# Performance work log

Measured on AMD Instinct MI355X. Metric: run time of the kernel, lower is better.

The kernel has to match this reference:

```python
import jax, jax.numpy as jnp
import numpy as np

EPS = 1e-5

def _ligru_layer(x, W, U, gamma, beta):
    # x: [B,T,F]; W: [2H,F]; U: [2H,H]; gamma/beta: [2H]
    B, T, _ = x.shape
    H = U.shape[1]
    w = jnp.einsum('btf,hf->bth', x, W)            # [B,T,2H] input projection
    # BatchNorm1d (training mode) over flattened (B*T, 2H)
    wf = w.reshape(B * T, 2 * H)
    mu = wf.mean(axis=0)
    var = wf.var(axis=0)
    wf = (wf - mu) / jnp.sqrt(var + EPS) * gamma + beta
    w = wf.reshape(B, T, 2 * H)

    Ut = U.T                                       # [H,2H]

    def step(h, wt):
        uh = h @ Ut                                # [B,2H]
        m = uh.mean(axis=-1, keepdims=True)
        v = uh.var(axis=-1, keepdims=True)
        uh = (uh - m) / jnp.sqrt(v + EPS)          # LayerNorm, no affine
        gates = wt + uh
        at, zt = gates[:, :H], gates[:, H:]
        zt = jax.nn.sigmoid(zt)
        h = zt * h + (1.0 - zt) * jax.nn.relu(at)
        return h, h

    h0 = jnp.zeros((B, H), x.dtype)
    _, hs = jax.lax.scan(step, h0, jnp.swapaxes(w, 0, 1))  # [T,B,H]
    return jnp.swapaxes(hs, 0, 1)                          # [B,T,H]


def setup_inputs() -> dict:
    key = jax.random.key(0)
    ks = jax.random.split(key, 5)
    B, T, F, H = 32, 1000, 80, 1024
    x = jax.random.normal(ks[0], (B, T, F), dtype=jnp.float32)
    W1 = jax.random.normal(ks[1], (2 * H, F), dtype=jnp.float32) * 0.05
    U1 = jax.random.normal(ks[2], (2 * H, H), dtype=jnp.float32) * 0.03
    W2 = jax.random.normal(ks[3], (2 * H, H), dtype=jnp.float32) * 0.03
    U2 = jax.random.normal(ks[4], (2 * H, H), dtype=jnp.float32) * 0.03
    g = jnp.ones((2 * H,), jnp.float32)
    b = jnp.zeros((2 * H,), jnp.float32)
    return {"x": x, "W1": W1, "U1": U1, "g1": g, "b1": b,
            "W2": W2, "U2": U2, "g2": g, "b2": b}


def reference(x, W1, U1, g1, b1, W2, U2, g2, b2):
    h = _ligru_layer(x, W1, U1, g1, b1)
    h = _ligru_layer(h, W2, U2, g2, b2)
    return h
```

## Files before the change

kernel.cpp:

```cpp
#include <hip/hip_runtime.h>

typedef unsigned short u16;
typedef _Float16 f16;
typedef f16 half8 __attribute__((ext_vector_type(8)));
typedef float float4v __attribute__((ext_vector_type(4)));

union HV { uint4 u; half8 h; u16 s[8]; };

__device__ __forceinline__ float h2f(u16 u) { union { u16 u; f16 h; } c; c.u = u; return (float)c.h; }
__device__ __forceinline__ u16 f2h(float f) { union { u16 u; f16 h; } c; c.h = (f16)f; return c.u; }

__device__ __forceinline__ void store_coh_u16(u16* p, unsigned v) {
  asm volatile("global_store_short %0, %1, off sc0 sc1" :: "v"(p), "v"(v) : "memory");
}
__device__ __forceinline__ void store_coh_u32(void* p, unsigned v) {
  asm volatile("global_store_dword %0, %1, off sc0 sc1" :: "v"(p), "v"(v) : "memory");
}
__device__ __forceinline__ void store_coh_f32_tag(float* p, float val, unsigned tag) {
  unsigned long long pk = (unsigned long long)__float_as_uint(val) |
                          ((unsigned long long)tag << 32);
  asm volatile("global_store_dwordx2 %0, %1, off sc0 sc1" :: "v"(p), "v"(pk) : "memory");
}

__global__ void cvt_f32_f16(const float* __restrict__ s, u16* __restrict__ d, int n) {
  for (int i = blockIdx.x * blockDim.x + threadIdx.x; i < n; i += gridDim.x * blockDim.x)
    d[i] = f2h(s[i]);
}

__global__ __launch_bounds__(256) void gemm_f16(const u16* __restrict__ A, const u16* __restrict__ B,
                                                u16* __restrict__ C, int K) {
  __shared__ u16 As[128][40];
  __shared__ u16 Bs[128][40];
  const int tid = threadIdx.x, lane = tid & 63, wid = tid >> 6;
  const int col = lane & 15, quad = lane >> 4;
  const int wm = (wid & 1) * 64, wn = (wid >> 1) * 64;
  const int n0 = blockIdx.x * 128;
  const int m0 = blockIdx.y * 128;
  float4v acc[4][4];
  #pragma unroll
  for (int i = 0; i < 4; ++i)
    #pragma unroll
    for (int j = 0; j < 4; ++j) acc[i][j] = (float4v){0.f, 0.f, 0.f, 0.f};

  const int srow = tid >> 2;
  const int schunk = (tid & 3) * 8;

  for (int k0 = 0; k0 < K; k0 += 32) {
    __syncthreads();
    #pragma unroll
    for (int r2 = 0; r2 < 2; ++r2) {
      int row = srow + 64 * r2;
      int kk = k0 + schunk;
      uint4 av = {0, 0, 0, 0}, bv = {0, 0, 0, 0};
      if (kk + 8 <= K) {
        av = *(const uint4*)(A + (size_t)(m0 + row) * K + kk);
        bv = *(const uint4*)(B + (size_t)(n0 + row) * K + kk);
      }
      *(uint4*)&As[row][schunk] = av;
      *(uint4*)&Bs[row][schunk] = bv;
    }
    __syncthreads();
    HV af[4], bf[4];
    #pragma unroll
    for (int i = 0; i < 4; ++i) af[i].u = *(const uint4*)&As[wm + i * 16 + col][quad * 8];
    #pragma unroll
    for (int j = 0; j < 4; ++j) bf[j].u = *(const uint4*)&Bs[wn + j * 16 + col][quad * 8];
    #pragma unroll
    for (int i = 0; i < 4; ++i)
      #pragma unroll
      for (int j = 0; j < 4; ++j)
        acc[i][j] = __builtin_amdgcn_mfma_f32_16x16x32_f16(af[i].h, bf[j].h, acc[i][j], 0, 0, 0);
  }
  #pragma unroll
  for (int i = 0; i < 4; ++i)
    #pragma unroll
    for (int j = 0; j < 4; ++j)
      #pragma unroll
      for (int r = 0; r < 4; ++r) {
        int m = m0 + wm + i * 16 + quad * 4 + r;
        int n = n0 + wn + j * 16 + col;
        C[(size_t)m * 2048 + n] = f2h(acc[i][j][r]);
      }
}

__global__ void bn_stats(const u16* __restrict__ C, float* __restrict__ acc) {
  int c = blockIdx.x * 256 + threadIdx.x;
  int r0 = blockIdx.y * 256;
  float s = 0.f, q = 0.f;
  for (int r = r0; r < r0 + 256; ++r) {
    float v = h2f(C[(size_t)r * 2048 + c]);
    s += v; q += v * v;
  }
  atomicAdd(&acc[2 * c], s);
  atomicAdd(&acc[2 * c + 1], q);
}

__global__ void bn_final(const float* __restrict__ acc, const float* __restrict__ g,
                         const float* __restrict__ b, float2* __restrict__ ss) {
  int c = blockIdx.x * 256 + threadIdx.x;
  float mean = acc[2 * c] * (1.f / 32000.f);
  float var = acc[2 * c + 1] * (1.f / 32000.f) - mean * mean;
  float sc = g[c] * rsqrtf(var + 1e-5f);
  float2 o; o.x = sc; o.y = b[c] - mean * sc;
  ss[c] = o;
}

template <int OUT_F32>
__global__ __launch_bounds__(256, 1) void rec_kernel(
    const u16* __restrict__ w,
    const float2* __restrict__ ss,
    const u16* __restrict__ U,
    u16* hbuf,
    float* pstats,
    unsigned* flags,
    u16* out16, float* out32) {
  const int tid = threadIdx.x, lane = tid & 63, kh = tid >> 6;
  const int d = blockIdx.x >> 5, beta = blockIdx.x & 31;
  const int col = lane & 15, quad = lane >> 4;
  __shared__ float4v red[3][4][64];

  const int ja = beta * 32 + col;

  HV ufA0[8], ufA1[8], ufZ0[8], ufZ1[8];
  #pragma unroll
  for (int kk = 0; kk < 8; ++kk) {
    int k = kh * 256 + kk * 32 + quad * 8;
    ufA0[kk].u = *(const uint4*)(U + (size_t)ja * 1024 + k);
    ufA1[kk].u = *(const uint4*)(U + (size_t)(ja + 16) * 1024 + k);
    ufZ0[kk].u = *(const uint4*)(U + (size_t)(1024 + ja) * 1024 + k);
    ufZ1[kk].u = *(const uint4*)(U + (size_t)(1024 + ja + 16) * 1024 + k);
  }
  float2 ssA0 = ss[ja], ssA1 = ss[ja + 16];
  float2 ssZ0 = ss[1024 + ja], ssZ1 = ss[1024 + ja + 16];

  u16* hb = hbuf + (size_t)d * 16 * 1024;
  float* ps = pstats + (size_t)d * 4096;
  unsigned* f2 = flags + (size_t)d * 512;

  const u16* aptr = hb + (size_t)col * 1024 + kh * 256 + quad * 8;
  const int bloc = quad * 4;

  float hreg[4][2] = {{0.f, 0.f}, {0.f, 0.f}, {0.f, 0.f}, {0.f, 0.f}};
  u16 wa0[4], wa1[4], wz0[4], wz1[4];
  if (kh == 0) {
    #pragma unroll
    for (int r = 0; r < 4; ++r) {
      const u16* wr = w + ((size_t)(d * 16 + bloc + r) * 1000 + 0) * 2048 + ja;
      wa0[r] = wr[0]; wa1[r] = wr[16]; wz0[r] = wr[1024]; wz1[r] = wr[1040];
    }
  }

  for (int t = 0; t < 1000; ++t) {
    const unsigned tag = (unsigned)t + 1u;
    HV af[8];
    asm volatile(
        "global_load_dwordx4 %0, %8, off sc0 sc1\n\t"
        "global_load_dwordx4 %1, %8, off offset:64  sc0 sc1\n\t"
        "global_load_dwordx4 %2, %8, off offset:128 sc0 sc1\n\t"
        "global_load_dwordx4 %3, %8, off offset:192 sc0 sc1\n\t"
        "global_load_dwordx4 %4, %8, off offset:256 sc0 sc1\n\t"
        "global_load_dwordx4 %5, %8, off offset:320 sc0 sc1\n\t"
        "global_load_dwordx4 %6, %8, off offset:384 sc0 sc1\n\t"
        "global_load_dwordx4 %7, %8, off offset:448 sc0 sc1\n\t"
        "s_waitcnt vmcnt(0)"
        : "=v"(af[0].u), "=v"(af[1].u), "=v"(af[2].u), "=v"(af[3].u),
          "=v"(af[4].u), "=v"(af[5].u), "=v"(af[6].u), "=v"(af[7].u)
        : "v"(aptr)
        : "memory");

    float4v aA0 = (float4v){0.f, 0.f, 0.f, 0.f};
    float4v aA1 = (float4v){0.f, 0.f, 0.f, 0.f};
    float4v aZ0 = (float4v){0.f, 0.f, 0.f, 0.f};
    float4v aZ1 = (float4v){0.f, 0.f, 0.f, 0.f};
    #pragma unroll
    for (int kk = 0; kk < 8; ++kk) {
      aA0 = __builtin_amdgcn_mfma_f32_16x16x32_f16(af[kk].h, ufA0[kk].h, aA0, 0, 0, 0);
      aA1 = __builtin_amdgcn_mfma_f32_16x16x32_f16(af[kk].h, ufA1[kk].h, aA1, 0, 0, 0);
      aZ0 = __builtin_amdgcn_mfma_f32_16x16x32_f16(af[kk].h, ufZ0[kk].h, aZ0, 0, 0, 0);
      aZ1 = __builtin_amdgcn_mfma_f32_16x16x32_f16(af[kk].h, ufZ1[kk].h, aZ1, 0, 0, 0);
    }
    if (kh) {
      red[kh - 1][0][lane] = aA0; red[kh - 1][1][lane] = aA1;
      red[kh - 1][2][lane] = aZ0; red[kh - 1][3][lane] = aZ1;
    }
    __syncthreads();

    if (kh == 0) {
      aA0 += red[0][0][lane] + red[1][0][lane] + red[2][0][lane];
      aA1 += red[0][1][lane] + red[1][1][lane] + red[2][1][lane];
      aZ0 += red[0][2][lane] + red[1][2][lane] + red[2][2][lane];
      aZ1 += red[0][3][lane] + red[1][3][lane] + red[2][3][lane];
      const int p = t & 1;
      #pragma unroll
      for (int r = 0; r < 4; ++r) {
        float sv = aA0[r] + aA1[r] + aZ0[r] + aZ1[r];
        float qv = aA0[r] * aA0[r] + aA1[r] * aA1[r] + aZ0[r] * aZ0[r] + aZ1[r] * aZ1[r];
        #pragma unroll
        for (int off = 1; off < 16; off <<= 1) {
          sv += __shfl_xor(sv, off, 64);
          qv += __shfl_xor(qv, off, 64);
        }
        if (col == 0) {
          float* dst = ps + (((size_t)p * 16 + bloc + r) * 32 + beta) * 4;
          store_coh_f32_tag(dst, sv, tag);
          store_coh_f32_tag(dst + 2, qv, tag);
        }
      }
      u16 wn_a0[4], wn_a1[4], wn_z0[4], wn_z1[4];
      {
        int tn = t < 999 ? t + 1 : t;
        #pragma unroll
        for (int r = 0; r < 4; ++r) {
          const u16* wr = w + ((size_t)(d * 16 + bloc + r) * 1000 + tn) * 2048 + ja;
          wn_a0[r] = wr[0]; wn_a1[r] = wr[16]; wn_z0[r] = wr[1024]; wn_z1[r] = wr[1040];
        }
      }
      float4v g[8];
      const float* rb = ps + ((size_t)p * 16 + bloc) * 128 + col * 4;
      int ok;
      do {
        asm volatile(
            "global_load_dwordx4 %0, %8, off sc0 sc1\n\t"
            "global_load_dwordx4 %1, %8, off offset:256  sc0 sc1\n\t"
            "global_load_dwordx4 %2, %8, off offset:512  sc0 sc1\n\t"
            "global_load_dwordx4 %3, %8, off offset:768  sc0 sc1\n\t"
            "global_load_dwordx4 %4, %8, off offset:1024 sc0 sc1\n\t"
            "global_load_dwordx4 %5, %8, off offset:1280 sc0 sc1\n\t"
            "global_load_dwordx4 %6, %8, off offset:1536 sc0 sc1\n\t"
            "global_load_dwordx4 %7, %8, off offset:1792 sc0 sc1\n\t"
            "s_waitcnt vmcnt(0)"
            : "=v"(g[0]), "=v"(g[1]), "=v"(g[2]), "=v"(g[3]),
              "=v"(g[4]), "=v"(g[5]), "=v"(g[6]), "=v"(g[7])
            : "v"(rb)
            : "memory");
        int okl = 1;
        #pragma unroll
        for (int i = 0; i < 8; ++i)
          okl &= (__float_as_uint(g[i][1]) == tag && __float_as_uint(g[i][3]) == tag) ? 1 : 0;
        ok = __all(okl);
      } while (!ok);

      #pragma unroll
      for (int r = 0; r < 4; ++r) {
        float sm = g[2 * r][0] + g[2 * r + 1][0];
        float sq = g[2 * r][2] + g[2 * r + 1][2];
        #pragma unroll
        for (int off = 1; off < 16; off <<= 1) {
          sm += __shfl_xor(sm, off, 64);
          sq += __shfl_xor(sq, off, 64);
        }
        float mean = sm * (1.f / 2048.f);
        float var = sq * (1.f / 2048.f) - mean * mean;
        float inv = rsqrtf(var + 1e-5f);
        float ga0 = h2f(wa0[r]) * ssA0.x + ssA0.y + (aA0[r] - mean) * inv;
        float ga1 = h2f(wa1[r]) * ssA1.x + ssA1.y + (aA1[r] - mean) * inv;
        float gz0 = h2f(wz0[r]) * ssZ0.x + ssZ0.y + (aZ0[r] - mean) * inv;
        float gz1 = h2f(wz1[r]) * ssZ1.x + ssZ1.y + (aZ1[r] - mean) * inv;
        float z0 = 1.f / (1.f + __expf(-gz0));
        float z1 = 1.f / (1.f + __expf(-gz1));
        float h0 = z0 * hreg[r][0] + (1.f - z0) * (ga0 > 0.f ? ga0 : 0.f);
        float h1 = z1 * hreg[r][1] + (1.f - z1) * (ga1 > 0.f ? ga1 : 0.f);
        hreg[r][0] = h0; hreg[r][1] = h1;
        u16* hp = hb + (size_t)(bloc + r) * 1024 + ja;
        store_coh_u16(hp, (unsigned)f2h(h0));
        store_coh_u16(hp + 16, (unsigned)f2h(h1));
      }
      #pragma unroll
      for (int r = 0; r < 4; ++r) {
        wa0[r] = wn_a0[r]; wa1[r] = wn_a1[r];
        wz0[r] = wn_z0[r]; wz1[r] = wn_z1[r];
      }
      asm volatile("s_waitcnt vmcnt(0)" ::: "memory");
      if (lane == 0) store_coh_u32(f2 + (size_t)beta * 16, tag);
      #pragma unroll
      for (int r = 0; r < 4; ++r) {
        size_t orow = ((size_t)(d * 16 + bloc + r) * 1000 + t) * 1024 + ja;
        if (OUT_F32) { out32[orow] = hreg[r][0]; out32[orow + 16] = hreg[r][1]; }
        else         { out16[orow] = f2h(hreg[r][0]); out16[orow + 16] = f2h(hreg[r][1]); }
      }
    }
    {
      unsigned fv = tag; int ok;
      do {
        if (lane < 32)
          asm volatile("global_load_dword %0, %1, off sc0 sc1\n\ts_waitcnt vmcnt(0)"
                       : "=v"(fv) : "v"(f2 + (size_t)lane * 16) : "memory");
        ok = __all(lane < 32 ? (int)(fv >= tag) : 1);
      } while (!ok);
    }
  }
}

extern "C" void kernel_launch(void* const* d_in, const int* in_sizes, int n_in,
                              void* d_out, int out_size, void* d_ws, size_t ws_size,
                              hipStream_t stream) {
  (void)in_sizes; (void)n_in; (void)out_size;
  const float* x  = (const float*)d_in[0];
  const float* W1 = (const float*)d_in[1];
  const float* U1 = (const float*)d_in[2];
  const float* g1 = (const float*)d_in[3];
  const float* b1 = (const float*)d_in[4];
  const float* W2 = (const float*)d_in[5];
  const float* U2 = (const float*)d_in[6];
  const float* g2 = (const float*)d_in[7];
  const float* b2 = (const float*)d_in[8];

  char* ws = (char*)d_ws;
  size_t o = 0;
  auto take = [&](size_t bytes) { size_t r = o; o = (o + bytes + 255) & ~(size_t)255; return r; };
  u16* wbuf  = (u16*)(ws + take(32000ULL * 2048 * 2));
  u16* h1seq = (u16*)(ws + take(32000ULL * 1024 * 2));
  u16* xb    = (u16*)(ws + take(32000ULL * 80 * 2));
  u16* W1b   = (u16*)(ws + take(2048ULL * 80 * 2));
  u16* W2b   = (u16*)(ws + take(2048ULL * 1024 * 2));
  u16* U1b   = (u16*)(ws + take(2048ULL * 1024 * 2));
  u16* U2b   = (u16*)(ws + take(2048ULL * 1024 * 2));
  float2* ss1 = (float2*)(ws + take(2048 * 8));
  float2* ss2 = (float2*)(ws + take(2048 * 8));
  size_t zbase = o;
  float* acc1 = (float*)(ws + take(2048 * 8));
  float* acc2 = (float*)(ws + take(2048 * 8));
  float* pstats1 = (float*)(ws + take(2ULL * 2 * 16 * 32 * 4 * 4));
  float* pstats2 = (float*)(ws + take(2ULL * 2 * 16 * 32 * 4 * 4));
  unsigned* flags1 = (unsigned*)(ws + take(2ULL * 32 * 16 * 4));
  unsigned* flags2 = (unsigned*)(ws + take(2ULL * 32 * 16 * 4));
  u16* hbuf1 = (u16*)(ws + take(32 * 1024 * 2));
  u16* hbuf2 = (u16*)(ws + take(32 * 1024 * 2));
  size_t zlen = o - zbase;
  if (ws_size < o) return;

  (void)hipMemsetAsync(ws + zbase, 0, zlen, stream);

  cvt_f32_f16<<<1280, 256, 0, stream>>>(x, xb, 32000 * 80);
  cvt_f32_f16<<<160, 256, 0, stream>>>(W1, W1b, 2048 * 80);
  cvt_f32_f16<<<1024, 256, 0, stream>>>(U1, U1b, 2048 * 1024);
  cvt_f32_f16<<<1024, 256, 0, stream>>>(W2, W2b, 2048 * 1024);
  cvt_f32_f16<<<1024, 256, 0, stream>>>(U2, U2b, 2048 * 1024);

  gemm_f16<<<dim3(16, 250), 256, 0, stream>>>(xb, W1b, wbuf, 80);
  bn_stats<<<dim3(8, 125), 256, 0, stream>>>(wbuf, acc1);
  bn_final<<<8, 256, 0, stream>>>(acc1, g1, b1, ss1);
  rec_kernel<0><<<64, 256, 0, stream>>>(wbuf, ss1, U1b, hbuf1, pstats1, flags1, h1seq, nullptr);

  gemm_f16<<<dim3(16, 250), 256, 0, stream>>>(h1seq, W2b, wbuf, 1024);
  bn_stats<<<dim3(8, 125), 256, 0, stream>>>(wbuf, acc2);
  bn_final<<<8, 256, 0, stream>>>(acc2, g2, b2, ss2);
  rec_kernel<1><<<64, 256, 0, stream>>>(wbuf, ss2, U2b, hbuf2, pstats2, flags2, nullptr, (float*)d_out);
}
```

Before: 12.95 ms.

## Spread recurrent epilogue across all four waves instead of wave zero

Each of the four waves now stores its partial MFMA accumulators to shared memory and all-reduces them, so every wave holds the full sums. Each wave then handles the LayerNorm stats, gate math, h update and output stores for one quad of four batch rows, rather than wave 0 doing all 16 rows serially. Per-wave flags (four per block) replace the single block flag, and the spin-wait checks all four with one dwordx4 load. The intent is to shorten the serial per-timestep critical path, at the cost of extra LDS reads and more flag traffic.

```diff
diff --git a/kernel.cpp b/kernel.cpp
--- a/kernel.cpp
+++ b/kernel.cpp
@@ -117,7 +117,9 @@
   const int tid = threadIdx.x, lane = tid & 63, kh = tid >> 6;
   const int d = blockIdx.x >> 5, beta = blockIdx.x & 31;
   const int col = lane & 15, quad = lane >> 4;
-  __shared__ float4v red[3][4][64];
+  const int act = (quad == kh);
+  const int bloc = kh * 4;
+  __shared__ float4v red[4][4][64];
 
   const int ja = beta * 32 + col;
 
@@ -138,11 +140,10 @@
   unsigned* f2 = flags + (size_t)d * 512;
 
   const u16* aptr = hb + (size_t)col * 1024 + kh * 256 + quad * 8;
-  const int bloc = quad * 4;
 
   float hreg[4][2] = {{0.f, 0.f}, {0.f, 0.f}, {0.f, 0.f}, {0.f, 0.f}};
   u16 wa0[4], wa1[4], wz0[4], wz1[4];
-  if (kh == 0) {
+  if (act) {
     #pragma unroll
     for (int r = 0; r < 4; ++r) {
       const u16* wr = w + ((size_t)(d * 16 + bloc + r) * 1000 + 0) * 2048 + ja;
@@ -179,18 +180,20 @@
       aZ0 = __builtin_amdgcn_mfma_f32_16x16x32_f16(af[kk].h, ufZ0[kk].h, aZ0, 0, 0, 0);
       aZ1 = __builtin_amdgcn_mfma_f32_16x16x32_f16(af[kk].h, ufZ1[kk].h, aZ1, 0, 0, 0);
     }
-    if (kh) {
-      red[kh - 1][0][lane] = aA0; red[kh - 1][1][lane] = aA1;
-      red[kh - 1][2][lane] = aZ0; red[kh - 1][3][lane] = aZ1;
-    }
+    red[kh][0][lane] = aA0; red[kh][1][lane] = aA1;
+    red[kh][2][lane] = aZ0; red[kh][3][lane] = aZ1;
     __syncthreads();
 
-    if (kh == 0) {
-      aA0 += red[0][0][lane] + red[1][0][lane] + red[2][0][lane];
-      aA1 += red[0][1][lane] + red[1][1][lane] + red[2][1][lane];
-      aZ0 += red[0][2][lane] + red[1][2][lane] + red[2][2][lane];
-      aZ1 += red[0][3][lane] + red[1][3][lane] + red[2][3][lane];
-      const int p = t & 1;
+    {
+      const int k1 = (kh + 1) & 3, k2 = (kh + 2) & 3, k3 = (kh + 3) & 3;
+      aA0 += red[k1][0][lane] + red[k2][0][lane] + red[k3][0][lane];
+      aA1 += red[k1][1][lane] + red[k2][1][lane] + red[k3][1][lane];
+      aZ0 += red[k1][2][lane] + red[k2][2][lane] + red[k3][2][lane];
+      aZ1 += red[k1][3][lane] + red[k2][3][lane] + red[k3][3][lane];
+    }
+    const int p = t & 1;
+    u16 wn_a0[4], wn_a1[4], wn_z0[4], wn_z1[4];
+    if (act) {
       #pragma unroll
       for (int r = 0; r < 4; ++r) {
         float sv = aA0[r] + aA1[r] + aZ0[r] + aZ1[r];
@@ -206,7 +209,6 @@
           store_coh_f32_tag(dst + 2, qv, tag);
         }
       }
-      u16 wn_a0[4], wn_a1[4], wn_z0[4], wn_z1[4];
       {
         int tn = t < 999 ? t + 1 : t;
         #pragma unroll
@@ -270,8 +272,10 @@
         wa0[r] = wn_a0[r]; wa1[r] = wn_a1[r];
         wz0[r] = wn_z0[r]; wz1[r] = wn_z1[r];
       }
-      asm volatile("s_waitcnt vmcnt(0)" ::: "memory");
-      if (lane == 0) store_coh_u32(f2 + (size_t)beta * 16, tag);
+    }
+    asm volatile("s_waitcnt vmcnt(0)" ::: "memory");
+    if (lane == 0) store_coh_u32(f2 + (size_t)beta * 16 + kh, tag);
+    if (act) {
       #pragma unroll
       for (int r = 0; r < 4; ++r) {
         size_t orow = ((size_t)(d * 16 + bloc + r) * 1000 + t) * 1024 + ja;
@@ -280,12 +284,12 @@
       }
     }
     {
-      unsigned fv = tag; int ok;
+      uint4 v; int ok;
       do {
         if (lane < 32)
-          asm volatile("global_load_dword %0, %1, off sc0 sc1\n\ts_waitcnt vmcnt(0)"
-                       : "=v"(fv) : "v"(f2 + (size_t)lane * 16) : "memory");
-        ok = __all(lane < 32 ? (int)(fv >= tag) : 1);
+          asm volatile("global_load_dwordx4 %0, %1, off sc0 sc1\n\ts_waitcnt vmcnt(0)"
+                       : "=v"(v) : "v"(f2 + (size_t)lane * 16) : "memory");
+        ok = __all(lane < 32 ? (int)(v.x >= tag && v.y >= tag && v.z >= tag && v.w >= tag) : 1);
       } while (!ok);
     }
   }
```

After: 18.18 ms. 1.4x slower.

## Halve recurrent-kernel block count by giving each block 64 hidden columns

Applied to the files above, without the earlier changes.

The recurrent kernel now runs 32 blocks instead of 64, and each block owns 64 hidden units per gate instead of 32. U is held in registers at twice the size, and eight MFMA accumulators run per k-step. This halves the number of peers in each per-timestep flag barrier and LayerNorm partial-stats exchange, which cuts global polling traffic and sync latency on the critical path. The w prefetch for the next timestep is removed and w is now loaded within the current step. The costs are higher register pressure, possible spills, and twice the per-block compute per step.

```diff
diff --git a/kernel.cpp b/kernel.cpp
--- a/kernel.cpp
+++ b/kernel.cpp
@@ -115,40 +115,37 @@
     unsigned* flags,
     u16* out16, float* out32) {
   const int tid = threadIdx.x, lane = tid & 63, kh = tid >> 6;
-  const int d = blockIdx.x >> 5, beta = blockIdx.x & 31;
+  const int d = blockIdx.x >> 4, beta = blockIdx.x & 15;
   const int col = lane & 15, quad = lane >> 4;
-  __shared__ float4v red[3][4][64];
-
-  const int ja = beta * 32 + col;
-
-  HV ufA0[8], ufA1[8], ufZ0[8], ufZ1[8];
+  __shared__ float4v red[3][8][64];
+
+  const int A0 = beta * 64;
+
+  HV ufA[4][8], ufZ[4][8];
   #pragma unroll
-  for (int kk = 0; kk < 8; ++kk) {
-    int k = kh * 256 + kk * 32 + quad * 8;
-    ufA0[kk].u = *(const uint4*)(U + (size_t)ja * 1024 + k);
-    ufA1[kk].u = *(const uint4*)(U + (size_t)(ja + 16) * 1024 + k);
-    ufZ0[kk].u = *(const uint4*)(U + (size_t)(1024 + ja) * 1024 + k);
-    ufZ1[kk].u = *(const uint4*)(U + (size_t)(1024 + ja + 16) * 1024 + k);
+  for (int g = 0; g < 4; ++g)
+    #pragma unroll
+    for (int kk = 0; kk < 8; ++kk) {
+      int k = kh * 256 + kk * 32 + quad * 8;
+      int ja = A0 + g * 16 + col;
+      ufA[g][kk].u = *(const uint4*)(U + (size_t)ja * 1024 + k);
+      ufZ[g][kk].u = *(const uint4*)(U + (size_t)(1024 + ja) * 1024 + k);
+    }
+  float2 ssA[4], ssZ[4];
+  #pragma unroll
+  for (int g = 0; g < 4; ++g) {
+    ssA[g] = ss[A0 + g * 16 + col];
+    ssZ[g] = ss[1024 + A0 + g * 16 + col];
   }
-  float2 ssA0 = ss[ja], ssA1 = ss[ja + 16];
-  float2 ssZ0 = ss[1024 + ja], ssZ1 = ss[1024 + ja + 16];
 
   u16* hb = hbuf + (size_t)d * 16 * 1024;
-  float* ps = pstats + (size_t)d * 4096;
-  unsigned* f2 = flags + (size_t)d * 512;
+  float* ps = pstats + (size_t)d * 2048;
+  unsigned* f2 = flags + (size_t)d * 256;
 
   const u16* aptr = hb + (size_t)col * 1024 + kh * 256 + quad * 8;
   const int bloc = quad * 4;
 
-  float hreg[4][2] = {{0.f, 0.f}, {0.f, 0.f}, {0.f, 0.f}, {0.f, 0.f}};
-  u16 wa0[4], wa1[4], wz0[4], wz1[4];
-  if (kh == 0) {
-    #pragma unroll
-    for (int r = 0; r < 4; ++r) {
-      const u16* wr = w + ((size_t)(d * 16 + bloc + r) * 1000 + 0) * 2048 + ja;
-      wa0[r] = wr[0]; wa1[r] = wr[16]; wz0[r] = wr[1024]; wz1[r] = wr[1040];
-    }
-  }
+  float hreg[4][4] = {};
 
   for (int t = 0; t < 1000; ++t) {
     const unsigned tag = (unsigned)t + 1u;
@@ -168,82 +165,87 @@
         : "v"(aptr)
         : "memory");
 
-    float4v aA0 = (float4v){0.f, 0.f, 0.f, 0.f};
-    float4v aA1 = (float4v){0.f, 0.f, 0.f, 0.f};
-    float4v aZ0 = (float4v){0.f, 0.f, 0.f, 0.f};
-    float4v aZ1 = (float4v){0.f, 0.f, 0.f, 0.f};
-    #pragma unroll
-    for (int kk = 0; kk < 8; ++kk) {
-      aA0 = __builtin_amdgcn_mfma_f32_16x16x32_f16(af[kk].h, ufA0[kk].h, aA0, 0, 0, 0);
-      aA1 = __builtin_amdgcn_mfma_f32_16x16x32_f16(af[kk].h, ufA1[kk].h, aA1, 0, 0, 0);
-      aZ0 = __builtin_amdgcn_mfma_f32_16x16x32_f16(af[kk].h, ufZ0[kk].h, aZ0, 0, 0, 0);
-      aZ1 = __builtin_amdgcn_mfma_f32_16x16x32_f16(af[kk].h, ufZ1[kk].h, aZ1, 0, 0, 0);
-    }
+    float4v aA[4], aZ[4];
+    #pragma unroll
+    for (int g = 0; g < 4; ++g) {
+      aA[g] = (float4v){0.f, 0.f, 0.f, 0.f};
+      aZ[g] = (float4v){0.f, 0.f, 0.f, 0.f};
+    }
+    #pragma unroll
+    for (int kk = 0; kk < 8; ++kk)
+      #pragma unroll
+      for (int g = 0; g < 4; ++g) {
+        aA[g] = __builtin_amdgcn_mfma_f32_16x16x32_f16(af[kk].h, ufA[g][kk].h, aA[g], 0, 0, 0);
+        aZ[g] = __builtin_amdgcn_mfma_f32_16x16x32_f16(af[kk].h, ufZ[g][kk].h, aZ[g], 0, 0, 0);
+      }
     if (kh) {
-      red[kh - 1][0][lane] = aA0; red[kh - 1][1][lane] = aA1;
-      red[kh - 1][2][lane] = aZ0; red[kh - 1][3][lane] = aZ1;
+      #pragma unroll
+      for (int g = 0; g < 4; ++g) {
+        red[kh - 1][g][lane] = aA[g];
+        red[kh - 1][4 + g][lane] = aZ[g];
+      }
     }
     __syncthreads();
 
     if (kh == 0) {
-      aA0 += red[0][0][lane] + red[1][0][lane] + red[2][0][lane];
-      aA1 += red[0][1][lane] + red[1][1][lane] + red[2][1][lane];
-      aZ0 += red[0][2][lane] + red[1][2][lane] + red[2][2][lane];
-      aZ1 += red[0][3][lane] + red[1][3][lane] + red[2][3][lane];
+      u16 wa[4][4], wz[4][4];
+      #pragma unroll
+      for (int r = 0; r < 4; ++r) {
+        const u16* wr = w + ((size_t)(d * 16 + bloc + r) * 1000 + t) * 2048 + A0 + col;
+        #pragma unroll
+        for (int g = 0; g < 4; ++g) { wa[r][g] = wr[g * 16]; wz[r][g] = wr[1024 + g * 16]; }
+      }
+      #pragma unroll
+      for (int s = 0; s < 3; ++s)
+        #pragma unroll
+        for (int g = 0; g < 4; ++g) {
+          aA[g] += red[s][g][lane];
+          aZ[g] += red[s][4 + g][lane];
+        }
       const int p = t & 1;
       #pragma unroll
       for (int r = 0; r < 4; ++r) {
-        float sv = aA0[r] + aA1[r] + aZ0[r] + aZ1[r];
-        float qv = aA0[r] * aA0[r] + aA1[r] * aA1[r] + aZ0[r] * aZ0[r] + aZ1[r] * aZ1[r];
+        float sv = 0.f, qv = 0.f;
+        #pragma unroll
+        for (int g = 0; g < 4; ++g) {
+          sv += aA[g][r] + aZ[g][r];
+          qv += aA[g][r] * aA[g][r] + aZ[g][r] * aZ[g][r];
+        }
         #pragma unroll
         for (int off = 1; off < 16; off <<= 1) {
           sv += __shfl_xor(sv, off, 64);
           qv += __shfl_xor(qv, off, 64);
         }
         if (col == 0) {
-          float* dst = ps + (((size_t)p * 16 + bloc + r) * 32 + beta) * 4;
+          float* dst = ps + (((size_t)p * 16 + bloc + r) * 16 + beta) * 4;
           store_coh_f32_tag(dst, sv, tag);
           store_coh_f32_tag(dst + 2, qv, tag);
         }
       }
-      u16 wn_a0[4], wn_a1[4], wn_z0[4], wn_z1[4];
-      {
-        int tn = t < 999 ? t + 1 : t;
-        #pragma unroll
-        for (int r = 0; r < 4; ++r) {
-          const u16* wr = w + ((size_t)(d * 16 + bloc + r) * 1000 + tn) * 2048 + ja;
-          wn_a0[r] = wr[0]; wn_a1[r] = wr[16]; wn_z0[r] = wr[1024]; wn_z1[r] = wr[1040];
-        }
-      }
-      float4v g[8];
-      const float* rb = ps + ((size_t)p * 16 + bloc) * 128 + col * 4;
+      float4v g4[4];
+      const float* rb = ps + ((size_t)p * 16 + bloc) * 64 + col * 4;
       int ok;
       do {
         asm volatile(
-            "global_load_dwordx4 %0, %8, off sc0 sc1\n\t"
-            "global_load_dwordx4 %1, %8, off offset:256  sc0 sc1\n\t"
-            "global_load_dwordx4 %2, %8, off offset:512  sc0 sc1\n\t"
-            "global_load_dwordx4 %3, %8, off offset:768  sc0 sc1\n\t"
-            "global_load_dwordx4 %4, %8, off offset:1024 sc0 sc1\n\t"
-            "global_load_dwordx4 %5, %8, off offset:1280 sc0 sc1\n\t"
-            "global_load_dwordx4 %6, %8, off offset:1536 sc0 sc1\n\t"
-            "global_load_dwordx4 %7, %8, off offset:1792 sc0 sc1\n\t"
+            "global_load_dwordx4 %0, %4, off sc0 sc1\n\t"
+            "global_load_dwordx4 %1, %4, off offset:256 sc0 sc1\n\t"
+            "global_load_dwordx4 %2, %4, off offset:512 sc0 sc1\n\t"
+            "global_load_dwordx4 %3, %4, off offset:768 sc0 sc1\n\t"
             "s_waitcnt vmcnt(0)"
-            : "=v"(g[0]), "=v"(g[1]), "=v"(g[2]), "=v"(g[3]),
-              "=v"(g[4]), "=v"(g[5]), "=v"(g[6]), "=v"(g[7])
+            : "=v"(g4[0]), "=v"(g4[1]), "=v"(g4[2]), "=v"(g4[3])
             : "v"(rb)
             : "memory");
         int okl = 1;
         #pragma unroll
-        for (int i = 0; i < 8; ++i)
-          okl &= (__float_as_uint(g[i][1]) == tag && __float_as_uint(g[i][3]) == tag) ? 1 : 0;
+        for (int i = 0; i < 4; ++i)
+          okl &= (__float_as_uint(g4[i][1]) == tag && __float_as_uint(g4[i][3]) == tag) ? 1 : 0;
         ok = __all(okl);
       } while (!ok);
 
       #pragma unroll
       for (int r = 0; r < 4; ++r) {
-        float sm = g[2 * r][0] + g[2 * r + 1][0];
-        float sq = g[2 * r][2] + g[2 * r + 1][2];
+        float sm = g4[r][0];
+        float sq = g4[r][2];
         #pragma unroll
         for (int off = 1; off < 16; off <<= 1) {
           sm += __shfl_xor(sm, off, 64);
@@ -252,40 +254,35 @@
         float mean = sm * (1.f / 2048.f);
         float var = sq * (1.f / 2048.f) - mean * mean;
         float inv = rsqrtf(var + 1e-5f);
-        float ga0 = h2f(wa0[r]) * ssA0.x + ssA0.y + (aA0[r] - mean) * inv;
-        float ga1 = h2f(wa1[r]) * ssA1.x + ssA1.y + (aA1[r] - mean) * inv;
-        float gz0 = h2f(wz0[r]) * ssZ0.x + ssZ0.y + (aZ0[r] - mean) * inv;
-        float gz1 = h2f(wz1[r]) * ssZ1.x + ssZ1.y + (aZ1[r] - mean) * inv;
-        float z0 = 1.f / (1.f + __expf(-gz0));
-        float z1 = 1.f / (1.f + __expf(-gz1));
-        float h0 = z0 * hreg[r][0] + (1.f - z0) * (ga0 > 0.f ? ga0 : 0.f);
-        float h1 = z1 * hreg[r][1] + (1.f - z1) * (ga1 > 0.f ? ga1 : 0.f);
-        hreg[r][0] = h0; hreg[r][1] = h1;
-        u16* hp = hb + (size_t)(bloc + r) * 1024 + ja;
-        store_coh_u16(hp, (unsigned)f2h(h0));
-        store_coh_u16(hp + 16, (unsigned)f2h(h1));
-      }
-      #pragma unroll
-      for (int r = 0; r < 4; ++r) {
-        wa0[r] = wn_a0[r]; wa1[r] = wn_a1[r];
-        wz0[r] = wn_z0[r]; wz1[r] = wn_z1[r];
+        #pragma unroll
+        for (int g = 0; g < 4; ++g) {
+          float ga = h2f(wa[r][g]) * ssA[g].x + ssA[g].y + (aA[g][r] - mean) * inv;
+          float gz = h2f(wz[r][g]) * ssZ[g].x + ssZ[g].y + (aZ[g][r] - mean) * inv;
+          float z = 1.f / (1.f + __expf(-gz));
+          float h = z * hreg[r][g] + (1.f - z) * (ga > 0.f ? ga : 0.f);
+          hreg[r][g] = h;
+          store_coh_u16(hb + (size_t)(bloc + r) * 1024 + A0 + g * 16 + col, (unsigned)f2h(h));
+        }
       }
       asm volatile("s_waitcnt vmcnt(0)" ::: "memory");
       if (lane == 0) store_coh_u32(f2 + (size_t)beta * 16, tag);
       #pragma unroll
       for (int r = 0; r < 4; ++r) {
-        size_t orow = ((size_t)(d * 16 + bloc + r) * 1000 + t) * 1024 + ja;
-        if (OUT_F32) { out32[orow] = hreg[r][0]; out32[orow + 16] = hreg[r][1]; }
-        else         { out16[orow] = f2h(hreg[r][0]); out16[orow + 16] = f2h(hreg[r][1]); }
+        size_t orow = ((size_t)(d * 16 + bloc + r) * 1000 + t) * 1024 + A0 + col;
+        #pragma unroll
+        for (int g = 0; g < 4; ++g) {
+          if (OUT_F32) out32[orow + g * 16] = hreg[r][g];
+          else         out16[orow + g * 16] = f2h(hreg[r][g]);
+        }
       }
     }
     {
       unsigned fv = tag; int ok;
       do {
-        if (lane < 32)
+        if (lane < 16)
           asm volatile("global_load_dword %0, %1, off sc0 sc1\n\ts_waitcnt vmcnt(0)"
                        : "=v"(fv) : "v"(f2 + (size_t)lane * 16) : "memory");
-        ok = __all(lane < 32 ? (int)(fv >= tag) : 1);
+        ok = __all(lane < 16 ? (int)(fv >= tag) : 1);
       } while (!ok);
     }
   }
@@ -320,10 +317,10 @@
   size_t zbase = o;
   float* acc1 = (float*)(ws + take(2048 * 8));
   float* acc2 = (float*)(ws + take(2048 * 8));
-  float* pstats1 = (float*)(ws + take(2ULL * 2 * 16 * 32 * 4 * 4));
-  float* pstats2 = (float*)(ws + take(2ULL * 2 * 16 * 32 * 4 * 4));
-  unsigned* flags1 = (unsigned*)(ws + take(2ULL * 32 * 16 * 4));
-  unsigned* flags2 = (unsigned*)(ws + take(2ULL * 32 * 16 * 4));
+  float* pstats1 = (float*)(ws + take(2ULL * 2 * 16 * 16 * 4 * 4));
+  float* pstats2 = (float*)(ws + take(2ULL * 2 * 16 * 16 * 4 * 4));
+  unsigned* flags1 = (unsigned*)(ws + take(2ULL * 16 * 16 * 4));
+  unsigned* flags2 = (unsigned*)(ws + take(2ULL * 16 * 16 * 4));
   u16* hbuf1 = (u16*)(ws + take(32 * 1024 * 2));
   u16* hbuf2 = (u16*)(ws + take(32 * 1024 * 2));
   size_t zlen = o - zbase;
@@ -340,10 +337,10 @@
   gemm_f16<<<dim3(16, 250), 256, 0, stream>>>(xb, W1b, wbuf, 80);
   bn_stats<<<dim3(8, 125), 256, 0, stream>>>(wbuf, acc1);
   bn_final<<<8, 256, 0, stream>>>(acc1, g1, b1, ss1);
-  rec_kernel<0><<<64, 256, 0, stream>>>(wbuf, ss1, U1b, hbuf1, pstats1, flags1, h1seq, nullptr);
+  rec_kernel<0><<<32, 256, 0, stream>>>(wbuf, ss1, U1b, hbuf1, pstats1, flags1, h1seq, nullptr);
 
   gemm_f16<<<dim3(16, 250), 256, 0, stream>>>(h1seq, W2b, wbuf, 1024);
   bn_stats<<<dim3(8, 125), 256, 0, stream>>>(wbuf, acc2);
   bn_final<<<8, 256, 0, stream>>>(acc2, g2, b2, ss2);
-  rec_kernel<1><<<64, 256, 0, stream>>>(wbuf, ss2, U2b, hbuf2, pstats2, flags2, nullptr, (float*)d_out);
-}
+  rec_kernel<1><<<32, 256, 0, stream>>>(wbuf, ss2, U2b, hbuf2, pstats2, flags2, nullptr, (float*)d_out);
+}
```

After: 16.00 ms. +23.5%, slower.
